# Optimization experiments

Measured on AMD Instinct MI355X. Metric: run time of the kernel, lower is better.

The kernel has to match this reference:

```python
import jax, jax.numpy as jnp
import numpy as np

V = 28996  # BERT_VOCAB_SIZE
D = 768    # input_size (BERT embedding dim)
H = 768    # hidden_size
B, T, S = 32, 48, 128


def setup_inputs() -> dict:
    key = jax.random.key(0)
    ks = jax.random.split(key, 10)
    w = lambda k, shape: jax.random.normal(k, shape, jnp.float32) * 0.02
    return {
        "x": jax.random.normal(ks[0], (B, T, D), jnp.float32),
        "hidden_state": jax.random.normal(ks[1], (B, H), jnp.float32),
        "encoder_attention": jax.random.normal(ks[2], (B, S, H), jnp.float32),
        # GRUCell params (torch layout: weight_ih (3H, D), weight_hh (3H, H))
        "W_ih": w(ks[3], (3 * H, D)), "W_hh": w(ks[4], (3 * H, H)),
        "b_ih": jnp.zeros((3 * H,), jnp.float32), "b_hh": jnp.zeros((3 * H,), jnp.float32),
        # prediction_layer
        "W_pred": w(ks[5], (V, H)), "b_pred": jnp.zeros((V,), jnp.float32),
        # decoder_att_linear
        "W_att": w(ks[6], (H, H)), "b_att": jnp.zeros((H,), jnp.float32),
        # decoder_attn_weighted_ctx
        "W_ctx": w(ks[7], (H, 2 * H)), "b_ctx": jnp.zeros((H,), jnp.float32),
    }


def reference(x, hidden_state, encoder_attention,
              W_ih, W_hh, b_ih, b_hh,
              W_pred, b_pred, W_att, b_att, W_ctx, b_ctx):
    def gru(xt, h):  # torch nn.GRUCell math
        gi = xt @ W_ih.T + b_ih  # (B, 3H)
        gh = h @ W_hh.T + b_hh
        i_r, i_z, i_n = jnp.split(gi, 3, axis=-1)
        h_r, h_z, h_n = jnp.split(gh, 3, axis=-1)
        r = jax.nn.sigmoid(i_r + h_r)
        z = jax.nn.sigmoid(i_z + h_z)
        n = jnp.tanh(i_n + r * h_n)
        return (1.0 - z) * n + z * h

    def step(h, xt):  # xt: (B, D)
        h = gru(xt, h)
        logits = h @ W_pred.T + b_pred                      # (B, V)
        a = h @ W_att.T + b_att                              # (B, H)
        scores = jax.nn.softmax(
            jnp.einsum('bh,bsh->bs', a, encoder_attention), axis=-1)
        ctx = jnp.einsum('bs,bsh->bh', scores, encoder_attention)
        h_new = jnp.tanh(jnp.concatenate([ctx, h], axis=-1) @ W_ctx.T + b_ctx)
        return h_new, logits

    xT = jnp.swapaxes(x, 0, 1)  # (T, B, D)
    _, logits = jax.lax.scan(step, hidden_state, xT)  # logits: (T, B, V)
    return jnp.swapaxes(logits, 0, 1)  # (B, T, V)
```

## Files before the change

kernel.cpp:

```cpp
#include <hip/hip_runtime.h>
#include <hip/hip_bf16.h>

using bf16 = __hip_bfloat16;

typedef __attribute__((ext_vector_type(8))) short short8;
typedef __attribute__((ext_vector_type(4))) float floatx4;

#define BB 32
#define TT 48
#define SS 128
#define HH 768
#define VV 28996

__device__ __forceinline__ float sigmoidf_(float x) { return 1.0f / (1.0f + expf(-x)); }
__device__ __forceinline__ float tanhf_(float x) {
    float xx = fminf(fmaxf(x, -15.0f), 15.0f);
    float e = expf(2.0f * xx);
    return (e - 1.0f) / (e + 1.0f);
}

__device__ __forceinline__ float ld1cg(const float* p) {
    return __hip_atomic_load((float*)p, __ATOMIC_RELAXED, __HIP_MEMORY_SCOPE_AGENT);
}
__device__ __forceinline__ float2 ld2cg(const float* p) {
    unsigned long long u = __hip_atomic_load((unsigned long long*)p,
                                             __ATOMIC_RELAXED, __HIP_MEMORY_SCOPE_AGENT);
    union { unsigned long long u; float2 f; } c; c.u = u; return c.f;
}
__device__ __forceinline__ void st1cg(float* p, float v) {
    __hip_atomic_store(p, v, __ATOMIC_RELAXED, __HIP_MEMORY_SCOPE_AGENT);
}

__device__ __forceinline__ void split1(float v, bf16& h, bf16& l) {
    h = (bf16)v;
    l = (bf16)(v - __bfloat162float(h));
}

#define XQ    294912
#define WIHQ  442368
#define EQ    786432
#define WC1Q  147456
#define WATS  589824

__global__ __launch_bounds__(256)
void split_ops(const float* __restrict__ x, const float* __restrict__ Wih,
               const float* __restrict__ E, const float* __restrict__ Wctx,
               const float* __restrict__ Watt,
               bf16* __restrict__ xh, bf16* __restrict__ xl,
               bf16* __restrict__ wihh, bf16* __restrict__ wihl,
               bf16* __restrict__ eh, bf16* __restrict__ el,
               bf16* __restrict__ wc1h, bf16* __restrict__ wc1l,
               bf16* __restrict__ wath, bf16* __restrict__ watl)
{
    int idx = blockIdx.x * 256 + threadIdx.x;
    if (idx < XQ + WIHQ + EQ) {
        const float* src; bf16 *dh, *dl; int off;
        if (idx < XQ)            { src = x;   dh = xh;   dl = xl;   off = idx; }
        else if (idx < XQ + WIHQ){ src = Wih; dh = wihh; dl = wihl; off = idx - XQ; }
        else                     { src = E;   dh = eh;   dl = el;   off = idx - XQ - WIHQ; }
        float4 v = ((const float4*)src)[off];
        union { bf16 b[4]; uint2 u; } oh, ol;
        split1(v.x, oh.b[0], ol.b[0]); split1(v.y, oh.b[1], ol.b[1]);
        split1(v.z, oh.b[2], ol.b[2]); split1(v.w, oh.b[3], ol.b[3]);
        ((uint2*)dh)[off] = oh.u; ((uint2*)dl)[off] = ol.u;
    } else if (idx < XQ + WIHQ + EQ + WC1Q) {
        int rem = idx - XQ - WIHQ - EQ;
        int j = rem / 192, c4 = rem - j * 192;
        float4 v = *(const float4*)(Wctx + (size_t)j * 1536 + 4 * c4);
        union { bf16 b[4]; uint2 u; } oh, ol;
        split1(v.x, oh.b[0], ol.b[0]); split1(v.y, oh.b[1], ol.b[1]);
        split1(v.z, oh.b[2], ol.b[2]); split1(v.w, oh.b[3], ol.b[3]);
        ((uint2*)wc1h)[rem] = oh.u; ((uint2*)wc1l)[rem] = ol.u;
    } else if (idx < XQ + WIHQ + EQ + WC1Q + WATS) {
        int rem = idx - XQ - WIHQ - EQ - WC1Q;
        int n = rem / 768, k = rem - n * 768;
        float v = Watt[(size_t)k * 768 + n];
        bf16 h, l; split1(v, h, l);
        wath[rem] = h; watl[rem] = l;
    }
}

__global__ __launch_bounds__(256)
void gbias_k(const float* __restrict__ E, const float* __restrict__ batt,
             float* __restrict__ gbias)
{
    int row = blockIdx.x * 4 + (threadIdx.x >> 6);
    int lane = threadIdx.x & 63;
    const float* er = E + (size_t)row * 768;
    float acc = 0.f;
#pragma unroll
    for (int i = 0; i < 12; ++i) acc += er[i * 64 + lane] * batt[i * 64 + lane];
#pragma unroll
    for (int d = 32; d > 0; d >>= 1) acc += __shfl_xor(acc, d);
    if (lane == 0) gbias[row] = acc;
}

#define WPQ 5567232
__global__ __launch_bounds__(256)
void conv_pred(const float* __restrict__ Wp, bf16* __restrict__ Wpb)
{
    int idx = blockIdx.x * 256 + threadIdx.x;
    if (idx >= WPQ) return;
    float4 v = ((const float4*)Wp)[idx];
    union { bf16 b[4]; uint2 u; } o;
    o.b[0] = (bf16)v.x; o.b[1] = (bf16)v.y; o.b[2] = (bf16)v.z; o.b[3] = (bf16)v.w;
    ((uint2*)Wpb)[idx] = o.u;
}

__global__ __launch_bounds__(256)
void gemm_split(const bf16* __restrict__ Ahi, const bf16* __restrict__ Alo, int lda,
                const bf16* __restrict__ Bhi, const bf16* __restrict__ Blo, int ldb,
                const float* __restrict__ bias,
                float* __restrict__ C, int ldc, int M, int N, int K)
{
    __shared__ __align__(16) char smem[65536];
    const int tid  = threadIdx.x;
    const int lane = tid & 63;
    const int widx = tid >> 6;
    const int wm = widx >> 1, wn = widx & 1;
    const int m0 = blockIdx.y * 128, n0 = blockIdx.x * 128;

    floatx4 acc[4][4];
    const floatx4 fzero = {0.f, 0.f, 0.f, 0.f};
#pragma unroll
    for (int i = 0; i < 4; ++i)
#pragma unroll
        for (int j = 0; j < 4; ++j) acc[i][j] = fzero;

    const int srow = tid >> 3, sslot = tid & 7;

    for (int kb = 0; kb < K; kb += 64) {
        __syncthreads();
        const bf16* mats[4] = {Ahi, Alo, Bhi, Blo};
#pragma unroll
        for (int mt = 0; mt < 4; ++mt) {
            const bf16* base = mats[mt];
            int ld   = (mt < 2) ? lda : ldb;
            int row0 = (mt < 2) ? m0 : n0;
#pragma unroll
            for (int r = 0; r < 4; ++r) {
                int row = r * 32 + srow;
                int c = sslot ^ (row & 7);
                const bf16* gp = base + (size_t)(row0 + row) * ld + kb + c * 8;
                char* lp = smem + mt * 16384 + r * 4096 + widx * 1024;
                __builtin_amdgcn_global_load_lds(
                    (const __attribute__((address_space(1))) void*)gp,
                    (__attribute__((address_space(3))) void*)lp, 16, 0, 0);
            }
        }
        __syncthreads();
#pragma unroll
        for (int kc = 0; kc < 2; ++kc) {
            short8 ah[4], al[4], bh[4], bl[4];
#pragma unroll
            for (int i = 0; i < 4; ++i) {
                int mrow = wm * 64 + i * 16 + (lane & 15);
                int nrow = wn * 64 + i * 16 + (lane & 15);
                int ca = kc * 4 + (lane >> 4);
                int sm = (ca ^ (mrow & 7)) * 16, sn = (ca ^ (nrow & 7)) * 16;
                ah[i] = *(const short8*)(smem +         mrow * 128 + sm);
                al[i] = *(const short8*)(smem + 16384 + mrow * 128 + sm);
                bh[i] = *(const short8*)(smem + 32768 + nrow * 128 + sn);
                bl[i] = *(const short8*)(smem + 49152 + nrow * 128 + sn);
            }
#pragma unroll
            for (int i = 0; i < 4; ++i)
#pragma unroll
                for (int j = 0; j < 4; ++j) {
                    acc[i][j] = __builtin_amdgcn_mfma_f32_16x16x32_bf16(ah[i], bh[j], acc[i][j], 0, 0, 0);
                    acc[i][j] = __builtin_amdgcn_mfma_f32_16x16x32_bf16(ah[i], bl[j], acc[i][j], 0, 0, 0);
                    acc[i][j] = __builtin_amdgcn_mfma_f32_16x16x32_bf16(al[i], bh[j], acc[i][j], 0, 0, 0);
                }
        }
    }
#pragma unroll
    for (int i = 0; i < 4; ++i) {
        int gm0 = m0 + wm * 64 + i * 16 + (lane >> 4) * 4;
#pragma unroll
        for (int j = 0; j < 4; ++j) {
            int gn = n0 + wn * 64 + j * 16 + (lane & 15);
            float bv = bias ? bias[gn] : 0.0f;
#pragma unroll
            for (int r2 = 0; r2 < 4; ++r2)
                C[(size_t)(gm0 + r2) * ldc + gn] = acc[i][j][r2] + bv;
        }
    }
}

__global__ __launch_bounds__(256)
void gemm_bt(const bf16* __restrict__ A, int lda,
             const bf16* __restrict__ Bm, int ldb,
             const float* __restrict__ bias,
             float* __restrict__ C, int ldc, int M, int N, int K)
{
    __shared__ __align__(16) char smem[32768];
    const int tid  = threadIdx.x;
    const int lane = tid & 63;
    const int widx = tid >> 6;
    const int wm = widx >> 1, wn = widx & 1;
    const int m0 = blockIdx.y * 128, n0 = blockIdx.x * 128;

    floatx4 acc[4][4];
    const floatx4 fzero = {0.f, 0.f, 0.f, 0.f};
#pragma unroll
    for (int i = 0; i < 4; ++i)
#pragma unroll
        for (int j = 0; j < 4; ++j) acc[i][j] = fzero;

    const int srow = tid >> 3, sslot = tid & 7;

    for (int kb = 0; kb < K; kb += 64) {
        __syncthreads();
#pragma unroll
        for (int r = 0; r < 4; ++r) {
            int mrow = r * 32 + srow;
            int c = sslot ^ (mrow & 7);
            const bf16* gp = A + (size_t)(m0 + mrow) * lda + kb + c * 8;
            char* lp = smem + r * 4096 + widx * 1024;
            __builtin_amdgcn_global_load_lds(
                (const __attribute__((address_space(1))) void*)gp,
                (__attribute__((address_space(3))) void*)lp, 16, 0, 0);
        }
#pragma unroll
        for (int r = 0; r < 4; ++r) {
            int nrow = r * 32 + srow;
            int gn = n0 + nrow; if (gn > N - 1) gn = N - 1;
            int c = sslot ^ (nrow & 7);
            const bf16* gp = Bm + (size_t)gn * ldb + kb + c * 8;
            char* lp = smem + 16384 + r * 4096 + widx * 1024;
            __builtin_amdgcn_global_load_lds(
                (const __attribute__((address_space(1))) void*)gp,
                (__attribute__((address_space(3))) void*)lp, 16, 0, 0);
        }
        __syncthreads();
#pragma unroll
        for (int kc = 0; kc < 2; ++kc) {
            short8 af[4], bfr[4];
#pragma unroll
            for (int i = 0; i < 4; ++i) {
                int mrow = wm * 64 + i * 16 + (lane & 15);
                int nrow = wn * 64 + i * 16 + (lane & 15);
                int ca = kc * 4 + (lane >> 4);
                af[i]  = *(const short8*)(smem +         mrow * 128 + ((ca ^ (mrow & 7)) * 16));
                bfr[i] = *(const short8*)(smem + 16384 + nrow * 128 + ((ca ^ (nrow & 7)) * 16));
            }
#pragma unroll
            for (int i = 0; i < 4; ++i)
#pragma unroll
                for (int j = 0; j < 4; ++j)
                    acc[i][j] = __builtin_amdgcn_mfma_f32_16x16x32_bf16(af[i], bfr[j], acc[i][j], 0, 0, 0);
        }
    }
#pragma unroll
    for (int i = 0; i < 4; ++i) {
        int gm0 = m0 + wm * 64 + i * 16 + (lane >> 4) * 4;
#pragma unroll
        for (int j = 0; j < 4; ++j) {
            int gn = n0 + wn * 64 + j * 16 + (lane & 15);
            if (gn < N) {
                float bv = bias ? bias[gn] : 0.0f;
#pragma unroll
                for (int r2 = 0; r2 < 4; ++r2)
                    C[(size_t)(gm0 + r2) * ldc + gn] = acc[i][j][r2] + bv;
            }
        }
    }
}

__global__ __launch_bounds__(256)
void transpose_f(const float* __restrict__ F, float* __restrict__ Ft)
{
    __shared__ float tile[32][33];
    int tx = threadIdx.x & 31, ty = threadIdx.x >> 5;
    int r0 = blockIdx.x << 5, j0 = blockIdx.y << 5;
#pragma unroll
    for (int i = 0; i < 4; ++i)
        tile[ty + 8 * i][tx] = F[(size_t)(r0 + ty + 8 * i) * 768 + j0 + tx];
    __syncthreads();
#pragma unroll
    for (int i = 0; i < 4; ++i)
        Ft[(size_t)(j0 + ty + 8 * i) * 4096 + r0 + tx] = tile[tx][ty + 8 * i];
}

#define NBARL 8
__device__ __forceinline__ void grid_barrier(unsigned int* bars, unsigned int target)
{
    __syncthreads();
    if (threadIdx.x == 0) {
        atomicAdd(&bars[(blockIdx.x & (NBARL - 1)) * 32], 1u);
        unsigned int s;
        do {
            __builtin_amdgcn_s_sleep(2);
            s = 0;
#pragma unroll
            for (int i = 0; i < NBARL; ++i)
                s += __hip_atomic_load(&bars[i * 32], __ATOMIC_RELAXED,
                                       __HIP_MEMORY_SCOPE_AGENT);
        } while (s < target);
    }
    __syncthreads();
}

__global__ __launch_bounds__(512)
void seq_coop(const float* __restrict__ gi,
              const float* __restrict__ G,
              const float* __restrict__ Ft,
              const float* __restrict__ gbias,
              const float* __restrict__ h0,
              const float* __restrict__ Whh,
              const float* __restrict__ Wctx,
              const float* __restrict__ bhh,
              const float* __restrict__ bctx,
              float* __restrict__ Ha,
              float* __restrict__ Hb,
              float* __restrict__ Sc,
              unsigned int* __restrict__ bar,
              bf16* __restrict__ Hseq)
{
    const int bid  = blockIdx.x;
    const int tid  = threadIdx.x;
    const int w    = tid >> 6;
    const int lane = tid & 63;
    const int kg   = lane & 7;
    const int bo   = lane >> 3;
    const int j0   = bid * 3;

    __shared__ __align__(16) float Wlds[12][768];
    __shared__ float part[8][9][32];
    __shared__ float redsum[9][32];
    __shared__ float c2s[3][32];
    __shared__ float pT[128][33];
    __shared__ float ctxp[3][4][32];

    for (int idx = tid; idx < 12 * 768; idx += 512) {
        int rr = idx / 768, k = idx - rr * 768;
        float v;
        if (rr < 9) {
            int gate = rr / 3, jj = rr - gate * 3;
            v = Whh[(size_t)(gate * 768 + j0 + jj) * 768 + k];
        } else {
            int jj = rr - 9;
            v = Wctx[(size_t)(j0 + jj) * 1536 + 768 + k];
        }
        (&Wlds[0][0])[idx] = v;
    }

    float bhr = 0.f, bhz = 0.f, bhn = 0.f, bcv = 0.f;
    if (tid < 96) {
        int jj = tid >> 5;
        bhr = bhh[j0 + jj]; bhz = bhh[768 + j0 + jj]; bhn = bhh[1536 + j0 + jj];
        bcv = bctx[j0 + jj];
    }
    const int bstar = bid >> 3;
    const int s0    = (bid & 7) * 16;
    const int k4b   = 3 * (8 * w + kg);

    unsigned int target = 256;
    __syncthreads();

#pragma unroll 1
    for (int t = 0; t < TT; ++t) {
        const float* hp = (t == 0) ? h0 : Ha;

        float e_ir = 0.f, e_iz = 0.f, e_inn = 0.f, e_hprev = 0.f;
        if (tid < 96) {
            int jj = tid >> 5, bb = tid & 31;
            const float* gir = gi + (size_t)(bb * TT + t) * 2304 + j0 + jj;
            e_ir = gir[0]; e_iz = gir[768]; e_inn = gir[1536];
            e_hprev = ld1cg(hp + bb * 768 + j0 + jj);
        }

        {
            float acc[9][4];
#pragma unroll
            for (int r = 0; r < 9; ++r)
#pragma unroll
                for (int q = 0; q < 4; ++q) acc[r][q] = 0.f;
            const float* hp_b = hp + bo * 768 + 4 * k4b;
            float2 h2[4][6];
#pragma unroll
            for (int q = 0; q < 4; ++q) {
                const float* hq = hp_b + q * 8 * 768;
#pragma unroll
                for (int i = 0; i < 6; ++i) h2[q][i] = ld2cg(hq + 2 * i);
            }
#pragma unroll
            for (int r = 0; r < 9; ++r) {
                const float* wr_ = &Wlds[r][4 * k4b];
#pragma unroll
                for (int i = 0; i < 6; ++i) {
                    float2 w2 = *(const float2*)(wr_ + 2 * i);
#pragma unroll
                    for (int q = 0; q < 4; ++q)
                        acc[r][q] += w2.x * h2[q][i].x + w2.y * h2[q][i].y;
                }
            }
#pragma unroll
            for (int r = 0; r < 9; ++r)
#pragma unroll
                for (int q = 0; q < 4; ++q) {
                    float v = acc[r][q];
                    v += __shfl_xor(v, 1); v += __shfl_xor(v, 2); v += __shfl_xor(v, 4);
                    if (kg == 0) part[w][r][bo + 8 * q] = v;
                }
        }
        __syncthreads();
        if (tid < 288) {
            int rr = tid >> 5, bb = tid & 31;
            float s = 0.f;
#pragma unroll
            for (int ww = 0; ww < 8; ++ww) s += part[ww][rr][bb];
            redsum[rr][bb] = s;
        }
        __syncthreads();
        if (tid < 96) {
            int jj = tid >> 5, bb = tid & 31;
            float r = sigmoidf_(e_ir + redsum[jj][bb] + bhr);
            float z = sigmoidf_(e_iz + redsum[3 + jj][bb] + bhz);
            float n = tanhf_(e_inn + r * (redsum[6 + jj][bb] + bhn));
            float ht = (1.f - z) * n + z * e_hprev;
            st1cg(&Hb[bb * 768 + j0 + jj], ht);
            Hseq[(size_t)(bb * TT + t) * 768 + j0 + jj] = (bf16)ht;
        }
        grid_barrier(bar, target); target += 256;

        {
            float a2[3][4];
#pragma unroll
            for (int c = 0; c < 3; ++c)
#pragma unroll
                for (int q = 0; q < 4; ++q) a2[c][q] = 0.f;
            const float* hb_b = Hb + bo * 768 + 4 * k4b;
            float2 h2[4][6];
#pragma unroll
            for (int q = 0; q < 4; ++q) {
                const float* hq = hb_b + q * 8 * 768;
#pragma unroll
                for (int i = 0; i < 6; ++i) h2[q][i] = ld2cg(hq + 2 * i);
            }
#pragma unroll
            for (int c = 0; c < 3; ++c) {
                const float* wr_ = &Wlds[9 + c][4 * k4b];
#pragma unroll
                for (int i = 0; i < 6; ++i) {
                    float2 w2 = *(const float2*)(wr_ + 2 * i);
#pragma unroll
                    for (int q = 0; q < 4; ++q)
                        a2[c][q] += w2.x * h2[q][i].x + w2.y * h2[q][i].y;
                }
            }
#pragma unroll
            for (int c = 0; c < 3; ++c)
#pragma unroll
                for (int q = 0; q < 4; ++q) {
                    float v = a2[c][q];
                    v += __shfl_xor(v, 1); v += __shfl_xor(v, 2); v += __shfl_xor(v, 4);
                    if (kg == 0) part[w][c][bo + 8 * q] = v;
                }
        }
        {
            const float* hb = Hb + bstar * 768;
            float2 a[6];
#pragma unroll
            for (int q = 0; q < 3; ++q) {
                a[2 * q]     = ld2cg(hb + 4 * (q * 64 + lane));
                a[2 * q + 1] = ld2cg(hb + 4 * (q * 64 + lane) + 2);
            }
#pragma unroll
            for (int ss = 0; ss < 2; ++ss) {
                const int s = s0 + 2 * w + ss;
                const float* grow = G + (size_t)(bstar * 128 + s) * 768;
                float sa = 0.f;
#pragma unroll
                for (int q = 0; q < 3; ++q) {
                    float4 g4 = *(const float4*)(grow + 4 * (q * 64 + lane));
                    sa += a[2 * q].x * g4.x + a[2 * q].y * g4.y
                        + a[2 * q + 1].x * g4.z + a[2 * q + 1].y * g4.w;
                }
#pragma unroll
                for (int d = 32; d > 0; d >>= 1) sa += __shfl_xor(sa, d);
                if (lane == 0)
                    st1cg(&Sc[bstar * 128 + s], sa + gbias[bstar * 128 + s]);
            }
        }
        grid_barrier(bar, target); target += 256;

        if (tid < 96) {
            int jj = tid >> 5, bb = tid & 31;
            float s = 0.f;
#pragma unroll
            for (int ww = 0; ww < 8; ++ww) s += part[ww][jj][bb];
            c2s[jj][bb] = s;
        }
        {
#pragma unroll
            for (int q = 0; q < 4; ++q) {
                int bb = 4 * w + q;
                float v0 = ld1cg(&Sc[bb * 128 + lane]);
                float v1 = ld1cg(&Sc[bb * 128 + 64 + lane]);
                float m = fmaxf(v0, v1);
#pragma unroll
                for (int d = 32; d > 0; d >>= 1) m = fmaxf(m, __shfl_xor(m, d));
                float e0 = expf(v0 - m), e1 = expf(v1 - m);
                float sum = e0 + e1;
#pragma unroll
                for (int d = 32; d > 0; d >>= 1) sum += __shfl_xor(sum, d);
                float inv = 1.f / sum;
                pT[lane][bb] = e0 * inv;
                pT[64 + lane][bb] = e1 * inv;
            }
        }
        __syncthreads();
        if (tid < 384) {
            int jj = tid >> 7, rem = tid & 127, sh = rem >> 5, bb = rem & 31;
            const float* fr = Ft + (size_t)(j0 + jj) * 4096 + bb * 128 + 32 * sh;
            float ca = 0.f;
#pragma unroll
            for (int q = 0; q < 8; ++q) {
                float4 f4 = *(const float4*)(fr + 4 * q);
                int sb = 32 * sh + 4 * q;
                ca += f4.x * pT[sb][bb] + f4.y * pT[sb + 1][bb]
                    + f4.z * pT[sb + 2][bb] + f4.w * pT[sb + 3][bb];
            }
            ctxp[jj][sh][bb] = ca;
        }
        __syncthreads();
        if (tid < 96) {
            int jj = tid >> 5, bb = tid & 31;
            float ctx = ctxp[jj][0][bb] + ctxp[jj][1][bb]
                      + ctxp[jj][2][bb] + ctxp[jj][3][bb];
            float u = c2s[jj][bb] + ctx + bcv;
            st1cg(&Ha[bb * 768 + j0 + jj], tanhf_(u));
        }
        grid_barrier(bar, target); target += 256;
    }
}

extern "C" void kernel_launch(void* const* d_in, const int* in_sizes, int n_in,
                              void* d_out, int out_size, void* d_ws, size_t ws_size,
                              hipStream_t stream)
{
    const float* x      = (const float*)d_in[0];
    const float* h0     = (const float*)d_in[1];
    const float* E      = (const float*)d_in[2];
    const float* W_ih   = (const float*)d_in[3];
    const float* W_hh   = (const float*)d_in[4];
    const float* b_ih   = (const float*)d_in[5];
    const float* b_hh   = (const float*)d_in[6];
    const float* W_pred = (const float*)d_in[7];
    const float* b_pred = (const float*)d_in[8];
    const float* W_att  = (const float*)d_in[9];
    const float* b_att  = (const float*)d_in[10];
    const float* W_ctx  = (const float*)d_in[11];
    const float* b_ctx  = (const float*)d_in[12];
    float* out = (float*)d_out;

    char* ws = (char*)d_ws;
    float* gi    = (float*)(ws);
    float* G     = (float*)(ws + 14155776);
    float* F     = (float*)(ws + 26738688);
    bf16*  xh    = (bf16*)(ws + 39321600);
    bf16*  xl    = (bf16*)(ws + 41680896);
    bf16*  wihh  = (bf16*)(ws + 44040192);
    bf16*  wihl  = (bf16*)(ws + 47579136);
    bf16*  eh    = (bf16*)(ws + 51118080);
    bf16*  el    = (bf16*)(ws + 57409536);
    bf16*  wath  = (bf16*)(ws + 63700992);
    bf16*  watl  = (bf16*)(ws + 64880640);
    bf16*  wc1h  = (bf16*)(ws + 66060288);
    bf16*  wc1l  = (bf16*)(ws + 67239936);
    bf16*  Hseq  = (bf16*)(ws + 68419584);
    float* gbias = (float*)(ws + 70778880);
    float* Ha    = (float*)(ws + 70795264);
    float* Hb    = (float*)(ws + 70893568);
    float* Sc    = (float*)(ws + 70991872);
    unsigned int* bar = (unsigned int*)(ws + 71008256);
    float* Ft    = (float*)(ws + 51118080);
    bf16*  Wpredb = (bf16*)(ws);

    hipMemsetAsync(bar, 0, NBARL * 32 * 4, stream);

    split_ops<<<8832, 256, 0, stream>>>(x, W_ih, E, W_ctx, W_att,
                                        xh, xl, wihh, wihl, eh, el,
                                        wc1h, wc1l, wath, watl);
    gbias_k<<<1024, 256, 0, stream>>>(E, b_att, gbias);

    gemm_split<<<dim3(18, 12), 256, 0, stream>>>(
        xh, xl, 768, wihh, wihl, 768, b_ih, gi, 2304, BB * TT, 2304, 768);
    gemm_split<<<dim3(6, 32), 256, 0, stream>>>(
        eh, el, 768, wath, watl, 768, nullptr, G, 768, BB * SS, 768, 768);
    gemm_split<<<dim3(6, 32), 256, 0, stream>>>(
        eh, el, 768, wc1h, wc1l, 768, nullptr, F, 768, BB * SS, 768, 768);
    transpose_f<<<dim3(128, 24), 256, 0, stream>>>(F, Ft);

    seq_coop<<<256, 512, 0, stream>>>(gi, G, Ft, gbias, h0, W_hh, W_ctx,
                                      b_hh, b_ctx, Ha, Hb, Sc, bar, Hseq);

    conv_pred<<<21747, 256, 0, stream>>>(W_pred, Wpredb);
    gemm_bt<<<dim3(227, 12), 256, 0, stream>>>(
        Hseq, 768, Wpredb, 768, b_pred, out, VV, BB * TT, VV, 768);
}
```

Baseline: 2.283 ms.

## Shrink recurrent cooperative grid to 96 blocks and drop one barrier per step

```diff
diff --git a/kernel.cpp b/kernel.cpp
--- a/kernel.cpp
+++ b/kernel.cpp
@@ -82,7 +82,7 @@
 
 __global__ __launch_bounds__(256)
 void gbias_k(const float* __restrict__ E, const float* __restrict__ batt,
-             float* __restrict__ gbias)
+             float* __restrict__ gbias, float* __restrict__ Sc0)
 {
     int row = blockIdx.x * 4 + (threadIdx.x >> 6);
     int lane = threadIdx.x & 63;
@@ -92,7 +92,7 @@
     for (int i = 0; i < 12; ++i) acc += er[i * 64 + lane] * batt[i * 64 + lane];
 #pragma unroll
     for (int d = 32; d > 0; d >>= 1) acc += __shfl_xor(acc, d);
-    if (lane == 0) gbias[row] = acc;
+    if (lane == 0) { gbias[row] = acc; st1cg(&Sc0[row], acc); }
 }
 
 #define WPQ 5567232
@@ -282,6 +282,7 @@
         Ft[(size_t)(j0 + ty + 8 * i) * 4096 + r0 + tx] = tile[tx][ty + 8 * i];
 }
 
+#define NBLK 96
 #define NBARL 8
 __device__ __forceinline__ void grid_barrier(unsigned int* bars, unsigned int target)
 {
@@ -290,7 +291,7 @@
         atomicAdd(&bars[(blockIdx.x & (NBARL - 1)) * 32], 1u);
         unsigned int s;
         do {
-            __builtin_amdgcn_s_sleep(2);
+            __builtin_amdgcn_s_sleep(1);
             s = 0;
 #pragma unroll
             for (int i = 0; i < NBARL; ++i)
@@ -303,7 +304,7 @@
 
 __global__ __launch_bounds__(512)
 void seq_coop(const float* __restrict__ gi,
-              const float* __restrict__ G,
+              const float* __restrict__ Gt,
               const float* __restrict__ Ft,
               const float* __restrict__ gbias,
               const float* __restrict__ h0,
@@ -323,47 +324,50 @@
     const int lane = tid & 63;
     const int kg   = lane & 7;
     const int bo   = lane >> 3;
-    const int j0   = bid * 3;
-
-    __shared__ __align__(16) float Wlds[12][768];
-    __shared__ float part[8][9][32];
-    __shared__ float redsum[9][32];
-    __shared__ float c2s[3][32];
-    __shared__ float pT[128][33];
-    __shared__ float ctxp[3][4][32];
-
-    for (int idx = tid; idx < 12 * 768; idx += 512) {
+    const int j0   = bid * 8;
+
+    __shared__ __align__(16) float Wlds[32][768];
+    __shared__ __align__(16) char  scr[24576];
+    __shared__ float partc2[8][8][32];
+    __shared__ float redsum[24][32];
+    __shared__ float h8[8][32];
+
+    float (*part)[24][32] = (float (*)[24][32])scr;
+    float (*pT)[33]       = (float (*)[33])scr;
+    float (*ctxp)[2][32]  = (float (*)[2][32])(scr + 16896);
+
+    for (int idx = tid; idx < 32 * 768; idx += 512) {
         int rr = idx / 768, k = idx - rr * 768;
         float v;
-        if (rr < 9) {
-            int gate = rr / 3, jj = rr - gate * 3;
+        if (rr < 24) {
+            int gate = rr >> 3, jj = rr & 7;
             v = Whh[(size_t)(gate * 768 + j0 + jj) * 768 + k];
         } else {
-            int jj = rr - 9;
+            int jj = rr - 24;
             v = Wctx[(size_t)(j0 + jj) * 1536 + 768 + k];
         }
         (&Wlds[0][0])[idx] = v;
     }
 
     float bhr = 0.f, bhz = 0.f, bhn = 0.f, bcv = 0.f;
-    if (tid < 96) {
+    if (tid < 256) {
         int jj = tid >> 5;
         bhr = bhh[j0 + jj]; bhz = bhh[768 + j0 + jj]; bhn = bhh[1536 + j0 + jj];
         bcv = bctx[j0 + jj];
     }
-    const int bstar = bid >> 3;
-    const int s0    = (bid & 7) * 16;
-    const int k4b   = 3 * (8 * w + kg);
-
-    unsigned int target = 256;
+    const int k4b = 3 * (8 * w + kg);
+
+    unsigned int target = NBLK;
     __syncthreads();
 
 #pragma unroll 1
     for (int t = 0; t < TT; ++t) {
         const float* hp = (t == 0) ? h0 : Ha;
+        float* Sc_cur = Sc + (t & 1) * (BB * SS);
+        float* Sc_nxt = Sc + ((t + 1) & 1) * (BB * SS);
 
         float e_ir = 0.f, e_iz = 0.f, e_inn = 0.f, e_hprev = 0.f;
-        if (tid < 96) {
+        if (tid < 256) {
             int jj = tid >> 5, bb = tid & 31;
             const float* gir = gi + (size_t)(bb * TT + t) * 2304 + j0 + jj;
             e_ir = gir[0]; e_iz = gir[768]; e_inn = gir[1536];
@@ -371,11 +375,6 @@
         }
 
         {
-            float acc[9][4];
-#pragma unroll
-            for (int r = 0; r < 9; ++r)
-#pragma unroll
-                for (int q = 0; q < 4; ++q) acc[r][q] = 0.f;
             const float* hp_b = hp + bo * 768 + 4 * k4b;
             float2 h2[4][6];
 #pragma unroll
@@ -385,51 +384,74 @@
                 for (int i = 0; i < 6; ++i) h2[q][i] = ld2cg(hq + 2 * i);
             }
 #pragma unroll
-            for (int r = 0; r < 9; ++r) {
-                const float* wr_ = &Wlds[r][4 * k4b];
-#pragma unroll
-                for (int i = 0; i < 6; ++i) {
-                    float2 w2 = *(const float2*)(wr_ + 2 * i);
-#pragma unroll
-                    for (int q = 0; q < 4; ++q)
-                        acc[r][q] += w2.x * h2[q][i].x + w2.y * h2[q][i].y;
+            for (int half = 0; half < 2; ++half) {
+                float acc[12][4];
+#pragma unroll
+                for (int r = 0; r < 12; ++r)
+#pragma unroll
+                    for (int q = 0; q < 4; ++q) acc[r][q] = 0.f;
+#pragma unroll
+                for (int r = 0; r < 12; ++r) {
+                    const float* wr_ = &Wlds[half * 12 + r][4 * k4b];
+#pragma unroll
+                    for (int i = 0; i < 6; ++i) {
+                        float2 w2 = *(const float2*)(wr_ + 2 * i);
+#pragma unroll
+                        for (int q = 0; q < 4; ++q)
+                            acc[r][q] += w2.x * h2[q][i].x + w2.y * h2[q][i].y;
+                    }
                 }
-            }
-#pragma unroll
-            for (int r = 0; r < 9; ++r)
-#pragma unroll
-                for (int q = 0; q < 4; ++q) {
-                    float v = acc[r][q];
-                    v += __shfl_xor(v, 1); v += __shfl_xor(v, 2); v += __shfl_xor(v, 4);
-                    if (kg == 0) part[w][r][bo + 8 * q] = v;
-                }
-        }
-        __syncthreads();
-        if (tid < 288) {
-            int rr = tid >> 5, bb = tid & 31;
+#pragma unroll
+                for (int r = 0; r < 12; ++r)
+#pragma unroll
+                    for (int q = 0; q < 4; ++q) {
+                        float v = acc[r][q];
+                        v += __shfl_xor(v, 1); v += __shfl_xor(v, 2); v += __shfl_xor(v, 4);
+                        if (kg == 0) part[w][half * 12 + r][bo + 8 * q] = v;
+                    }
+            }
+        }
+        __syncthreads();
+        for (int o = tid; o < 768; o += 512) {
+            int rr = o >> 5, bb = o & 31;
             float s = 0.f;
 #pragma unroll
             for (int ww = 0; ww < 8; ++ww) s += part[ww][rr][bb];
             redsum[rr][bb] = s;
         }
         __syncthreads();
-        if (tid < 96) {
+        if (tid < 256) {
             int jj = tid >> 5, bb = tid & 31;
             float r = sigmoidf_(e_ir + redsum[jj][bb] + bhr);
-            float z = sigmoidf_(e_iz + redsum[3 + jj][bb] + bhz);
-            float n = tanhf_(e_inn + r * (redsum[6 + jj][bb] + bhn));
+            float z = sigmoidf_(e_iz + redsum[8 + jj][bb] + bhz);
+            float n = tanhf_(e_inn + r * (redsum[16 + jj][bb] + bhn));
             float ht = (1.f - z) * n + z * e_hprev;
             st1cg(&Hb[bb * 768 + j0 + jj], ht);
             Hseq[(size_t)(bb * TT + t) * 768 + j0 + jj] = (bf16)ht;
-        }
-        grid_barrier(bar, target); target += 256;
-
+            h8[jj][bb] = ht;
+        }
+        __syncthreads();
         {
-            float a2[3][4];
-#pragma unroll
-            for (int c = 0; c < 3; ++c)
-#pragma unroll
-                for (int q = 0; q < 4; ++q) a2[c][q] = 0.f;
+            int bb = tid >> 4, so = tid & 15;
+            const float* gt0 = Gt + (size_t)j0 * 4096 + bb * 128 + so * 8;
+            float p[8];
+#pragma unroll
+            for (int si = 0; si < 8; ++si) p[si] = 0.f;
+#pragma unroll
+            for (int jj = 0; jj < 8; ++jj) {
+                float hv = h8[jj][bb];
+                float4 g0 = *(const float4*)(gt0 + (size_t)jj * 4096);
+                float4 g1 = *(const float4*)(gt0 + (size_t)jj * 4096 + 4);
+                p[0] += hv * g0.x; p[1] += hv * g0.y; p[2] += hv * g0.z; p[3] += hv * g0.w;
+                p[4] += hv * g1.x; p[5] += hv * g1.y; p[6] += hv * g1.z; p[7] += hv * g1.w;
+            }
+            float* scp = Sc_cur + bb * 128 + so * 8;
+#pragma unroll
+            for (int si = 0; si < 8; ++si) atomicAdd(scp + si, p[si]);
+        }
+        grid_barrier(bar, target); target += NBLK;
+
+        {
             const float* hb_b = Hb + bo * 768 + 4 * k4b;
             float2 h2[4][6];
 #pragma unroll
@@ -438,66 +460,37 @@
 #pragma unroll
                 for (int i = 0; i < 6; ++i) h2[q][i] = ld2cg(hq + 2 * i);
             }
-#pragma unroll
-            for (int c = 0; c < 3; ++c) {
-                const float* wr_ = &Wlds[9 + c][4 * k4b];
+            float a2[8][4];
+#pragma unroll
+            for (int r = 0; r < 8; ++r)
+#pragma unroll
+                for (int q = 0; q < 4; ++q) a2[r][q] = 0.f;
+#pragma unroll
+            for (int r = 0; r < 8; ++r) {
+                const float* wr_ = &Wlds[24 + r][4 * k4b];
 #pragma unroll
                 for (int i = 0; i < 6; ++i) {
                     float2 w2 = *(const float2*)(wr_ + 2 * i);
 #pragma unroll
                     for (int q = 0; q < 4; ++q)
-                        a2[c][q] += w2.x * h2[q][i].x + w2.y * h2[q][i].y;
+                        a2[r][q] += w2.x * h2[q][i].x + w2.y * h2[q][i].y;
                 }
             }
 #pragma unroll
-            for (int c = 0; c < 3; ++c)
+            for (int r = 0; r < 8; ++r)
 #pragma unroll
                 for (int q = 0; q < 4; ++q) {
-                    float v = a2[c][q];
+                    float v = a2[r][q];
                     v += __shfl_xor(v, 1); v += __shfl_xor(v, 2); v += __shfl_xor(v, 4);
-                    if (kg == 0) part[w][c][bo + 8 * q] = v;
+                    if (kg == 0) partc2[w][r][bo + 8 * q] = v;
                 }
-        }
-        {
-            const float* hb = Hb + bstar * 768;
-            float2 a[6];
-#pragma unroll
-            for (int q = 0; q < 3; ++q) {
-                a[2 * q]     = ld2cg(hb + 4 * (q * 64 + lane));
-                a[2 * q + 1] = ld2cg(hb + 4 * (q * 64 + lane) + 2);
-            }
-#pragma unroll
-            for (int ss = 0; ss < 2; ++ss) {
-                const int s = s0 + 2 * w + ss;
-                const float* grow = G + (size_t)(bstar * 128 + s) * 768;
-                float sa = 0.f;
-#pragma unroll
-                for (int q = 0; q < 3; ++q) {
-                    float4 g4 = *(const float4*)(grow + 4 * (q * 64 + lane));
-                    sa += a[2 * q].x * g4.x + a[2 * q].y * g4.y
-                        + a[2 * q + 1].x * g4.z + a[2 * q + 1].y * g4.w;
-                }
-#pragma unroll
-                for (int d = 32; d > 0; d >>= 1) sa += __shfl_xor(sa, d);
-                if (lane == 0)
-                    st1cg(&Sc[bstar * 128 + s], sa + gbias[bstar * 128 + s]);
-            }
-        }
-        grid_barrier(bar, target); target += 256;
-
-        if (tid < 96) {
-            int jj = tid >> 5, bb = tid & 31;
-            float s = 0.f;
-#pragma unroll
-            for (int ww = 0; ww < 8; ++ww) s += part[ww][jj][bb];
-            c2s[jj][bb] = s;
         }
         {
 #pragma unroll
             for (int q = 0; q < 4; ++q) {
                 int bb = 4 * w + q;
-                float v0 = ld1cg(&Sc[bb * 128 + lane]);
-                float v1 = ld1cg(&Sc[bb * 128 + 64 + lane]);
+                float v0 = ld1cg(&Sc_cur[bb * 128 + lane]);
+                float v1 = ld1cg(&Sc_cur[bb * 128 + 64 + lane]);
                 float m = fmaxf(v0, v1);
 #pragma unroll
                 for (int d = 32; d > 0; d >>= 1) m = fmaxf(m, __shfl_xor(m, d));
@@ -511,28 +504,36 @@
             }
         }
         __syncthreads();
-        if (tid < 384) {
-            int jj = tid >> 7, rem = tid & 127, sh = rem >> 5, bb = rem & 31;
-            const float* fr = Ft + (size_t)(j0 + jj) * 4096 + bb * 128 + 32 * sh;
+        float c2v = 0.f;
+        {
+            int jjc = tid >> 5, bbc = tid & 31;
+            if (tid < 256) {
+#pragma unroll
+                for (int ww = 0; ww < 8; ++ww) c2v += partc2[ww][jjc][bbc];
+            }
+        }
+        {
+            int jj = tid >> 6, sh = (tid >> 5) & 1, bb = tid & 31;
+            const float* fr = Ft + (size_t)(j0 + jj) * 4096 + bb * 128 + 64 * sh;
             float ca = 0.f;
 #pragma unroll
-            for (int q = 0; q < 8; ++q) {
-                float4 f4 = *(const float4*)(fr + 4 * q);
-                int sb = 32 * sh + 4 * q;
+            for (int qq = 0; qq < 16; ++qq) {
+                float4 f4 = *(const float4*)(fr + 4 * qq);
+                int sb = 64 * sh + 4 * qq;
                 ca += f4.x * pT[sb][bb] + f4.y * pT[sb + 1][bb]
                     + f4.z * pT[sb + 2][bb] + f4.w * pT[sb + 3][bb];
             }
             ctxp[jj][sh][bb] = ca;
         }
-        __syncthreads();
-        if (tid < 96) {
+        if (bid < 32 && tid < 128)
+            st1cg(&Sc_nxt[bid * 128 + tid], gbias[bid * 128 + tid]);
+        __syncthreads();
+        if (tid < 256) {
             int jj = tid >> 5, bb = tid & 31;
-            float ctx = ctxp[jj][0][bb] + ctxp[jj][1][bb]
-                      + ctxp[jj][2][bb] + ctxp[jj][3][bb];
-            float u = c2s[jj][bb] + ctx + bcv;
+            float u = c2v + ctxp[jj][0][bb] + ctxp[jj][1][bb] + bcv;
             st1cg(&Ha[bb * 768 + j0 + jj], tanhf_(u));
         }
-        grid_barrier(bar, target); target += 256;
+        grid_barrier(bar, target); target += NBLK;
     }
 }
 
@@ -574,8 +575,9 @@
     float* Ha    = (float*)(ws + 70795264);
     float* Hb    = (float*)(ws + 70893568);
     float* Sc    = (float*)(ws + 70991872);
-    unsigned int* bar = (unsigned int*)(ws + 71008256);
+    unsigned int* bar = (unsigned int*)(ws + 71024640);
     float* Ft    = (float*)(ws + 51118080);
+    float* Gt    = (float*)(ws + 26738688);
     bf16*  Wpredb = (bf16*)(ws);
 
     hipMemsetAsync(bar, 0, NBARL * 32 * 4, stream);
@@ -583,7 +585,7 @@
     split_ops<<<8832, 256, 0, stream>>>(x, W_ih, E, W_ctx, W_att,
                                         xh, xl, wihh, wihl, eh, el,
                                         wc1h, wc1l, wath, watl);
-    gbias_k<<<1024, 256, 0, stream>>>(E, b_att, gbias);
+    gbias_k<<<1024, 256, 0, stream>>>(E, b_att, gbias, Sc);
 
     gemm_split<<<dim3(18, 12), 256, 0, stream>>>(
         xh, xl, 768, wihh, wihl, 768, b_ih, gi, 2304, BB * TT, 2304, 768);
@@ -592,9 +594,10 @@
     gemm_split<<<dim3(6, 32), 256, 0, stream>>>(
         eh, el, 768, wc1h, wc1l, 768, nullptr, F, 768, BB * SS, 768, 768);
     transpose_f<<<dim3(128, 24), 256, 0, stream>>>(F, Ft);
-
-    seq_coop<<<256, 512, 0, stream>>>(gi, G, Ft, gbias, h0, W_hh, W_ctx,
-                                      b_hh, b_ctx, Ha, Hb, Sc, bar, Hseq);
+    transpose_f<<<dim3(128, 24), 256, 0, stream>>>(G, Gt);
+
+    seq_coop<<<NBLK, 512, 0, stream>>>(gi, Gt, Ft, gbias, h0, W_hh, W_ctx,
+                                       b_hh, b_ctx, Ha, Hb, Sc, bar, Hseq);
 
     conv_pred<<<21747, 256, 0, stream>>>(W_pred, Wpredb);
     gemm_bt<<<dim3(227, 12), 256, 0, stream>>>(
```

After: 4.314 ms. +89.0%, slower.
